# Kernel optimization log

Hardware: AMD Instinct MI355X
Metric: run time of the kernel (lower is better)

Reference implementation:

```python
import jax, jax.numpy as jnp
import numpy as np

N_NODES = 50000
N_EDGES = 800000
D_FEAT = 128
EPS = 1e-12  # torch F.normalize eps


def setup_inputs() -> dict:
    key = jax.random.key(0)
    k1, k2, k3 = jax.random.split(key, 3)
    feat = jax.random.normal(k1, (N_NODES, D_FEAT), dtype=jnp.float32)
    beta = jnp.ones((1,), dtype=jnp.float32)
    src = jax.random.randint(k2, (N_EDGES,), 0, N_NODES, dtype=jnp.int32)
    dst = jax.random.randint(k3, (N_EDGES,), 0, N_NODES, dtype=jnp.int32)
    return {"feat": feat, "beta": beta, "src": src, "dst": dst}


def reference(feat, beta, src, dst):
    # L2-normalize node features (F.normalize: x / max(||x||, eps))
    norm = jnp.maximum(jnp.linalg.norm(feat, axis=-1, keepdims=True), EPS)
    norm_h = feat / norm                                   # [N, D]
    # per-edge cosine similarity: u_dot_v
    cos = jnp.sum(norm_h[src] * norm_h[dst], axis=-1)      # [E]
    e = beta[0] * cos                                      # [E]
    # edge softmax over incoming edges of each destination node
    m = jax.ops.segment_max(e, dst, num_segments=N_NODES)  # [N]
    m = jax.lax.stop_gradient(m)
    e_exp = jnp.exp(e - m[dst])                            # [E]
    denom = jax.ops.segment_sum(e_exp, dst, num_segments=N_NODES)  # [N]
    p = e_exp / denom[dst]                                 # [E]
    # weighted sum aggregation: u_mul_e -> sum over incoming edges
    msgs = feat[src] * p[:, None]                          # [E, D]
    out = jax.ops.segment_sum(msgs, dst, num_segments=N_NODES)     # [N, D]
    return out
```

## Files before the change

kernel.cpp:

```cpp
#include <hip/hip_runtime.h>

#define N_NODES 50000
#define N_EDGES 800000
#define D_FEAT  128
#define EPS     1e-12f
#define CAP     64

#define NR          125
#define RANGE_NODES 400
#define RANGE_CAP   8192
#define A_BLOCKS    ((N_EDGES + 1023) / 1024)
#define ANORM_BLOCKS ((N_NODES + 31) / 32)

__device__ __forceinline__ unsigned int f2bf(float x) {
    unsigned int u = __float_as_uint(x);
    return (u + 0x7FFFu + ((u >> 16) & 1u)) >> 16;
}
__device__ __forceinline__ float bf_lo(unsigned int w) {
    return __uint_as_float(w << 16);
}
__device__ __forceinline__ float bf_hi(unsigned int w) {
    return __uint_as_float(w & 0xFFFF0000u);
}
__device__ __forceinline__ float dot2_bf16(unsigned int a, unsigned int b,
                                           float c) {
    float d;
    asm("v_dot2_f32_bf16 %0, %1, %2, %3"
        : "=v"(d) : "v"(a), "v"(b), "v"(c));
    return d;
}

__global__ void zero_cursor_kernel(int* __restrict__ cursor) {
    if (threadIdx.x < NR) cursor[threadIdx.x] = 0;
}

__global__ __launch_bounds__(1024) void partition_norm_kernel(
        const int* __restrict__ src,
        const int* __restrict__ dst,
        int* __restrict__ cursor,
        unsigned int* __restrict__ area,
        const float* __restrict__ feat,
        float* __restrict__ inv_norm,
        unsigned int* __restrict__ feat_bf) {
    __shared__ int hist[NR];
    __shared__ int base[NR];
    const int b = blockIdx.x;
    if (b < A_BLOCKS) {
        const int t = threadIdx.x;
        for (int i = t; i < NR; i += 1024) hist[i] = 0;
        __syncthreads();
        const int e = b * 1024 + t;
        int r = 0, lrank = 0;
        unsigned int w = 0;
        if (e < N_EDGES) {
            const int d = dst[e];
            r = d / RANGE_NODES;
            const int dl = d - r * RANGE_NODES;
            w = ((unsigned int)dl << 16) | (unsigned int)src[e];
            lrank = atomicAdd(&hist[r], 1);
        }
        __syncthreads();
        for (int i = t; i < NR; i += 1024)
            base[i] = atomicAdd(&cursor[i], hist[i]);
        __syncthreads();
        if (e < N_EDGES) {
            const int pos = base[r] + lrank;
            if (pos < RANGE_CAP)
                area[r * RANGE_CAP + pos] = w;
        }
        return;
    }
    const int nb  = b - A_BLOCKS;
    const int g   = threadIdx.x >> 5;
    const int sub = threadIdx.x & 31;
    const int node = nb * 32 + g;
    if (node >= N_NODES) return;
    float4 v = reinterpret_cast<const float4*>(feat + (size_t)node * D_FEAT)[sub];
    unsigned int w0 = (f2bf(v.y) << 16) | f2bf(v.x);
    unsigned int w1 = (f2bf(v.w) << 16) | f2bf(v.z);
    *reinterpret_cast<uint2*>(feat_bf + (size_t)node * 64 + sub * 2) =
        make_uint2(w0, w1);
    float s = v.x * v.x + v.y * v.y + v.z * v.z + v.w * v.w;
    #pragma unroll
    for (int off = 16; off > 0; off >>= 1)
        s += __shfl_xor(s, off, 64);
    if (sub == 0) {
        inv_norm[node] = 1.0f / fmaxf(sqrtf(s), EPS);
    }
}

__global__ __launch_bounds__(256) void rank_kernel(
        const int* __restrict__ cursor,
        const unsigned int* __restrict__ area,
        int* __restrict__ counts,
        unsigned short* __restrict__ bucket) {
    __shared__ int hist[RANGE_NODES];
    const int r = blockIdx.x, t = threadIdx.x;
    for (int i = t; i < RANGE_NODES; i += 256) hist[i] = 0;
    __syncthreads();
    const int nE = min(cursor[r], RANGE_CAP);
    const unsigned int* ra = area + r * RANGE_CAP;
    for (int i = t; i < nE; i += 256) {
        const unsigned int w = ra[i];
        const int dl = (int)(w >> 16);
        const int slot = atomicAdd(&hist[dl], 1);
        if (slot < CAP)
            bucket[(size_t)(r * RANGE_NODES + dl) * CAP + slot] =
                (unsigned short)(w & 0xFFFFu);
    }
    __syncthreads();
    for (int i = t; i < RANGE_NODES; i += 256)
        counts[r * RANGE_NODES + i] = hist[i];
}

__global__ void fused_agg(const unsigned int* __restrict__ feat_bf,
                          const float* __restrict__ inv_norm,
                          const int* __restrict__ counts,
                          const unsigned short* __restrict__ bucket,
                          const float* __restrict__ beta,
                          float* __restrict__ out) {
    const int lane = threadIdx.x & 63;
    const int grp  = lane >> 4;
    const int sub  = lane & 15;
    const int node = blockIdx.x * (blockDim.x >> 6) + (threadIdx.x >> 6);
    if (node >= N_NODES) return;

    const int cnt = min(counts[node], CAP);
    float4* orow = reinterpret_cast<float4*>(out + (size_t)node * D_FEAT);
    if (cnt == 0) {
        if (grp == 0) {
            orow[2 * sub] = make_float4(0.f, 0.f, 0.f, 0.f);
            orow[2 * sub + 1] = make_float4(0.f, 0.f, 0.f, 0.f);
        }
        return;
    }

    uint4 qd = reinterpret_cast<const uint4*>(feat_bf + (size_t)node * 64)[sub];
    const float bscale = inv_norm[node] * beta[0];

    float acc[8] = {0, 0, 0, 0, 0, 0, 0, 0};
    float denom = 0.0f;

    const int myid = (int)bucket[node * CAP + min(lane, cnt - 1)];

    const int s0 = __shfl(myid, min(grp, cnt - 1), 64);
    uint4 q0 = reinterpret_cast<const uint4*>(feat_bf + (size_t)s0 * 64)[sub];
    float in0 = inv_norm[s0];

    uint4 q1 = make_uint4(0u, 0u, 0u, 0u);
    float in1 = 0.0f;
    if (4 < cnt) {
        const int s1 = __shfl(myid, min(4 + grp, cnt - 1), 64);
        q1 = reinterpret_cast<const uint4*>(feat_bf + (size_t)s1 * 64)[sub];
        in1 = inv_norm[s1];
    }

    for (int k0 = 0; k0 < cnt; k0 += 4) {
        uint4 q2 = make_uint4(0u, 0u, 0u, 0u);
        float in2 = 0.0f;
        if (k0 + 8 < cnt) {
            const int s2 = __shfl(myid, min(k0 + 8 + grp, cnt - 1), 64);
            q2 = reinterpret_cast<const uint4*>(feat_bf + (size_t)s2 * 64)[sub];
            in2 = inv_norm[s2];
        }

        float dot = dot2_bf16(q0.x, qd.x, 0.0f);
        dot = dot2_bf16(q0.y, qd.y, dot);
        dot = dot2_bf16(q0.z, qd.z, dot);
        dot = dot2_bf16(q0.w, qd.w, dot);
        #pragma unroll
        for (int off = 8; off > 0; off >>= 1)
            dot += __shfl_xor(dot, off, 64);

        const bool valid = (k0 + grp) < cnt;
        const float ee = valid ? __expf(dot * (bscale * in0)) : 0.0f;

        float a[8];
        a[0] = bf_lo(q0.x); a[1] = bf_hi(q0.x);
        a[2] = bf_lo(q0.y); a[3] = bf_hi(q0.y);
        a[4] = bf_lo(q0.z); a[5] = bf_hi(q0.z);
        a[6] = bf_lo(q0.w); a[7] = bf_hi(q0.w);
        #pragma unroll
        for (int j = 0; j < 8; ++j) acc[j] += ee * a[j];
        denom += ee;

        q0 = q1; in0 = in1;
        q1 = q2; in1 = in2;
    }

    #pragma unroll
    for (int j = 0; j < 8; ++j) {
        acc[j] += __shfl_xor(acc[j], 16, 64);
        acc[j] += __shfl_xor(acc[j], 32, 64);
    }
    denom += __shfl_xor(denom, 16, 64);
    denom += __shfl_xor(denom, 32, 64);

    if (grp == 0) {
        const float scale = 1.0f / denom;
        orow[2 * sub] = make_float4(acc[0] * scale, acc[1] * scale,
                                    acc[2] * scale, acc[3] * scale);
        orow[2 * sub + 1] = make_float4(acc[4] * scale, acc[5] * scale,
                                        acc[6] * scale, acc[7] * scale);
    }
}

extern "C" void kernel_launch(void* const* d_in, const int* in_sizes, int n_in,
                              void* d_out, int out_size, void* d_ws, size_t ws_size,
                              hipStream_t stream) {
    const float* feat = (const float*)d_in[0];
    const float* beta = (const float*)d_in[1];
    const int*   src  = (const int*)d_in[2];
    const int*   dst  = (const int*)d_in[3];
    float* out = (float*)d_out;

    float*          inv_norm = (float*)d_ws;
    int*            counts   = (int*)(inv_norm + N_NODES);
    int*            cursor   = counts + N_NODES;
    unsigned int*   area     = (unsigned int*)(cursor + 128);
    unsigned short* bucket   = (unsigned short*)(area + (size_t)NR * RANGE_CAP);
    unsigned int*   feat_bf  = (unsigned int*)(bucket + (size_t)N_NODES * CAP);

    zero_cursor_kernel<<<1, 128, 0, stream>>>(cursor);
    partition_norm_kernel<<<A_BLOCKS + ANORM_BLOCKS, 1024, 0, stream>>>(
        src, dst, cursor, area, feat, inv_norm, feat_bf);
    rank_kernel<<<NR, 256, 0, stream>>>(cursor, area, counts, bucket);
    {
        const int WPB = 4;
        int blocks = (N_NODES + WPB - 1) / WPB;
        fused_agg<<<blocks, WPB * 64, 0, stream>>>(feat_bf, inv_norm, counts,
                                                   bucket, beta, out);
    }
}
```

Measured before the change: 81.00 us.

## Replace global-atomic edge partition with per-block local scan and block-info table

Each partition block now sorts its edges by destination range locally, using a shared-memory prefix scan, and writes them into its own slice of the staging area. It also records a per-range (offset,count) table, replacing global atomics on a shared cursor array and removing the zeroing kernel launch. The rank kernel then walks the per-block segments for its range, with each thread serially looping over one block's segment. This drops contention on global atomics and one launch. In exchange, the rank kernel gets irregular, poorly coalesced reads: each thread handles about 6-7 entries per block over 782 blocks.

```diff
diff --git a/kernel.cpp b/kernel.cpp
--- a/kernel.cpp
+++ b/kernel.cpp
@@ -8,8 +8,7 @@
 
 #define NR          125
 #define RANGE_NODES 400
-#define RANGE_CAP   8192
-#define A_BLOCKS    ((N_EDGES + 1023) / 1024)
+#define NBLK        ((N_EDGES + 1023) / 1024)
 #define ANORM_BLOCKS ((N_NODES + 31) / 32)
 
 __device__ __forceinline__ unsigned int f2bf(float x) {
@@ -30,29 +29,27 @@
     return d;
 }
 
-__global__ void zero_cursor_kernel(int* __restrict__ cursor) {
-    if (threadIdx.x < NR) cursor[threadIdx.x] = 0;
-}
-
 __global__ __launch_bounds__(1024) void partition_norm_kernel(
         const int* __restrict__ src,
         const int* __restrict__ dst,
-        int* __restrict__ cursor,
         unsigned int* __restrict__ area,
+        unsigned int* __restrict__ blkinfo,
         const float* __restrict__ feat,
         float* __restrict__ inv_norm,
         unsigned int* __restrict__ feat_bf) {
     __shared__ int hist[NR];
+    __shared__ int scan[128];
     __shared__ int base[NR];
     const int b = blockIdx.x;
-    if (b < A_BLOCKS) {
+    if (b < NBLK) {
         const int t = threadIdx.x;
-        for (int i = t; i < NR; i += 1024) hist[i] = 0;
+        if (t < NR) hist[t] = 0;
         __syncthreads();
         const int e = b * 1024 + t;
         int r = 0, lrank = 0;
         unsigned int w = 0;
-        if (e < N_EDGES) {
+        const bool ok = (e < N_EDGES);
+        if (ok) {
             const int d = dst[e];
             r = d / RANGE_NODES;
             const int dl = d - r * RANGE_NODES;
@@ -60,17 +57,24 @@
             lrank = atomicAdd(&hist[r], 1);
         }
         __syncthreads();
-        for (int i = t; i < NR; i += 1024)
-            base[i] = atomicAdd(&cursor[i], hist[i]);
-        __syncthreads();
-        if (e < N_EDGES) {
-            const int pos = base[r] + lrank;
-            if (pos < RANGE_CAP)
-                area[r * RANGE_CAP + pos] = w;
-        }
+        if (t < 128) scan[t] = (t < NR) ? hist[t] : 0;
+        __syncthreads();
+        for (int off = 1; off < 128; off <<= 1) {
+            int v = (t < 128 && t >= off) ? scan[t - off] : 0;
+            __syncthreads();
+            if (t < 128) scan[t] += v;
+            __syncthreads();
+        }
+        if (t < NR) base[t] = scan[t] - hist[t];
+        __syncthreads();
+        if (ok)
+            area[b * 1024 + base[r] + lrank] = w;
+        if (t < NR)
+            blkinfo[t * NBLK + b] =
+                ((unsigned int)base[t] << 16) | (unsigned int)hist[t];
         return;
     }
-    const int nb  = b - A_BLOCKS;
+    const int nb  = b - NBLK;
     const int g   = threadIdx.x >> 5;
     const int sub = threadIdx.x & 31;
     const int node = nb * 32 + g;
@@ -89,27 +93,31 @@
     }
 }
 
-__global__ __launch_bounds__(256) void rank_kernel(
-        const int* __restrict__ cursor,
+__global__ __launch_bounds__(512) void rank_kernel(
+        const unsigned int* __restrict__ blkinfo,
         const unsigned int* __restrict__ area,
         int* __restrict__ counts,
         unsigned short* __restrict__ bucket) {
     __shared__ int hist[RANGE_NODES];
     const int r = blockIdx.x, t = threadIdx.x;
-    for (int i = t; i < RANGE_NODES; i += 256) hist[i] = 0;
+    for (int i = t; i < RANGE_NODES; i += 512) hist[i] = 0;
     __syncthreads();
-    const int nE = min(cursor[r], RANGE_CAP);
-    const unsigned int* ra = area + r * RANGE_CAP;
-    for (int i = t; i < nE; i += 256) {
-        const unsigned int w = ra[i];
-        const int dl = (int)(w >> 16);
-        const int slot = atomicAdd(&hist[dl], 1);
-        if (slot < CAP)
-            bucket[(size_t)(r * RANGE_NODES + dl) * CAP + slot] =
-                (unsigned short)(w & 0xFFFFu);
+    const unsigned int* col = blkinfo + (size_t)r * NBLK;
+    for (int b = t; b < NBLK; b += 512) {
+        const unsigned int info = col[b];
+        const int cnt = (int)(info & 0xFFFFu);
+        const unsigned int* p = area + b * 1024 + (info >> 16);
+        for (int j = 0; j < cnt; ++j) {
+            const unsigned int w = p[j];
+            const int dl = (int)(w >> 16);
+            const int slot = atomicAdd(&hist[dl], 1);
+            if (slot < CAP)
+                bucket[(size_t)(r * RANGE_NODES + dl) * CAP + slot] =
+                    (unsigned short)(w & 0xFFFFu);
+        }
     }
     __syncthreads();
-    for (int i = t; i < RANGE_NODES; i += 256)
+    for (int i = t; i < RANGE_NODES; i += 512)
         counts[r * RANGE_NODES + i] = hist[i];
 }
 
@@ -141,7 +149,7 @@
     float acc[8] = {0, 0, 0, 0, 0, 0, 0, 0};
     float denom = 0.0f;
 
-    const int myid = (int)bucket[node * CAP + min(lane, cnt - 1)];
+    const int myid = (int)bucket[(size_t)node * CAP + min(lane, cnt - 1)];
 
     const int s0 = __shfl(myid, min(grp, cnt - 1), 64);
     uint4 q0 = reinterpret_cast<const uint4*>(feat_bf + (size_t)s0 * 64)[sub];
@@ -216,15 +224,14 @@
 
     float*          inv_norm = (float*)d_ws;
     int*            counts   = (int*)(inv_norm + N_NODES);
-    int*            cursor   = counts + N_NODES;
-    unsigned int*   area     = (unsigned int*)(cursor + 128);
-    unsigned short* bucket   = (unsigned short*)(area + (size_t)NR * RANGE_CAP);
+    unsigned int*   blkinfo  = (unsigned int*)(counts + N_NODES);
+    unsigned int*   area     = blkinfo + (size_t)NR * NBLK;
+    unsigned short* bucket   = (unsigned short*)(area + (size_t)NBLK * 1024);
     unsigned int*   feat_bf  = (unsigned int*)(bucket + (size_t)N_NODES * CAP);
 
-    zero_cursor_kernel<<<1, 128, 0, stream>>>(cursor);
-    partition_norm_kernel<<<A_BLOCKS + ANORM_BLOCKS, 1024, 0, stream>>>(
-        src, dst, cursor, area, feat, inv_norm, feat_bf);
-    rank_kernel<<<NR, 256, 0, stream>>>(cursor, area, counts, bucket);
+    partition_norm_kernel<<<NBLK + ANORM_BLOCKS, 1024, 0, stream>>>(
+        src, dst, area, blkinfo, feat, inv_norm, feat_bf);
+    rank_kernel<<<NR, 512, 0, stream>>>(blkinfo, area, counts, bucket);
     {
         const int WPB = 4;
         int blocks = (N_NODES + WPB - 1) / WPB;
```

After: 79.81 us. No clear change (-1.5%).
